# Optimization experiments

Measured on AMD Instinct MI355X. Metric: run time of the kernel, lower is better.

## Reference

```python
import jax, jax.numpy as jnp
import numpy as np


def gcn_layer(x, src, dst, W, b, n_dst):
    # DGL GraphConv, norm='both': D_src^{-1/2} pre-norm, sum aggregate, D_dst^{-1/2} post-norm, + bias
    n_src = x.shape[0]
    e_ones = jnp.ones(src.shape[0], dtype=x.dtype)
    deg_out = jnp.clip(jax.ops.segment_sum(e_ones, src, num_segments=n_src), 1.0)
    deg_in = jnp.clip(jax.ops.segment_sum(e_ones, dst, num_segments=n_dst), 1.0)
    h = (x * jax.lax.rsqrt(deg_out)[:, None]) @ W          # [n_src, out]
    agg = jax.ops.segment_sum(h[src], dst, num_segments=n_dst)  # [n_dst, out]
    return jax.nn.relu(agg * jax.lax.rsqrt(deg_in)[:, None] + b)


def setup_inputs() -> dict:
    key = jax.random.key(0)
    ks = jax.random.split(key, 8)
    N_SRC0, N_DST0, N_DST1 = 400000, 40000, 4000
    E0, E1 = 400000, 40000
    D_IN, D_HID, D_OUT = 256, 256, 256
    x = jax.random.normal(ks[0], (N_SRC0, D_IN), dtype=jnp.float32)
    src0 = jax.random.randint(ks[1], (E0,), 0, N_SRC0)
    dst0 = jax.random.randint(ks[2], (E0,), 0, N_DST0)
    src1 = jax.random.randint(ks[3], (E1,), 0, N_DST0)
    dst1 = jax.random.randint(ks[4], (E1,), 0, N_DST1)
    W0 = jax.random.normal(ks[5], (D_IN, D_HID), dtype=jnp.float32) * (1.0 / np.sqrt(D_IN))
    W1 = jax.random.normal(ks[6], (D_HID, D_OUT), dtype=jnp.float32) * (1.0 / np.sqrt(D_HID))
    b0 = jnp.zeros((D_HID,), dtype=jnp.float32)
    b1 = jnp.zeros((D_OUT,), dtype=jnp.float32)
    return {"x": x, "src0": src0, "dst0": dst0, "src1": src1, "dst1": dst1,
            "W0": W0, "b0": b0, "W1": W1, "b1": b1,
            "n_dst0": N_DST0, "n_dst1": N_DST1}


def reference(x, src0, dst0, src1, dst1, W0, b0, W1, b1, n_dst0, n_dst1):
    h = gcn_layer(x, src0, dst0, W0, b0, n_dst0)   # [n_dst0, hidden]
    out = gcn_layer(h, src1, dst1, W1, b1, n_dst1)  # [n_dst1, out]
    return out
```

## Files before the change

kernel.cpp:

```cpp
#include <hip/hip_runtime.h>
#include <hip/hip_bf16.h>
#include <cstddef>
#include <cstdint>


#define D 256
#define N_DST0_CONST 40000

typedef __attribute__((ext_vector_type(8))) short s16x8;
typedef __attribute__((ext_vector_type(4))) short s16x4;
typedef __attribute__((ext_vector_type(4))) float f32x4;

__device__ inline short f2bf(float f) {
    __hip_bfloat16 h = __float2bfloat16(f);
    return *reinterpret_cast<short*>(&h);
}

__global__ void zero_i(int* __restrict__ p, int n) {
    int i = blockIdx.x * blockDim.x + threadIdx.x;
    int stride = gridDim.x * blockDim.x;
    for (; i < n; i += stride) p[i] = 0;
}

__global__ void count_deg(const int* __restrict__ src, const int* __restrict__ dst,
                          int* __restrict__ cnt_src, int* __restrict__ cnt_dst, int E) {
    int e = blockIdx.x * blockDim.x + threadIdx.x;
    if (e < E) {
        atomicAdd(&cnt_src[src[e]], 1);
        atomicAdd(&cnt_dst[dst[e]], 1);
    }
}

__global__ void finalize_rsqrt(const int* __restrict__ cnt, float* __restrict__ rnorm, int n) {
    int i = blockIdx.x * blockDim.x + threadIdx.x;
    if (i < n) rnorm[i] = rsqrtf(fmaxf((float)cnt[i], 1.0f));
}

__global__ __launch_bounds__(1024) void ex_scan(const int* __restrict__ cnt,
                                                int* __restrict__ ptr, int n) {
    __shared__ int wsum[16];
    const int tid = threadIdx.x;
    const int chunk = (n + 1023) / 1024;
    const int begin = tid * chunk;
    const int end = min(begin + chunk, n);
    int local = 0;
    for (int i = begin; i < end; ++i) local += cnt[i];
    const int lane = tid & 63;
    const int wid = tid >> 6;
    int v = local;
    for (int off = 1; off < 64; off <<= 1) {
        int u = __shfl_up(v, off, 64);
        if (lane >= off) v += u;
    }
    if (lane == 63) wsum[wid] = v;
    __syncthreads();
    if (wid == 0 && lane < 16) {
        int w = wsum[lane];
        for (int off = 1; off < 16; off <<= 1) {
            int u = __shfl_up(w, off, 16);
            if (lane >= off) w += u;
        }
        wsum[lane] = w;
    }
    __syncthreads();
    int base = (wid > 0 ? wsum[wid - 1] : 0) + (v - local);
    int run = base;
    for (int i = begin; i < end; ++i) { ptr[i] = run; run += cnt[i]; }
}

__global__ void fill_csr(const int* __restrict__ src, const int* __restrict__ dst,
                         int* __restrict__ ptr, int* __restrict__ edge_src, int E) {
    int e = blockIdx.x * blockDim.x + threadIdx.x;
    if (e < E) {
        int pos = atomicAdd(&ptr[dst[e]], 1);
        edge_src[pos] = src[e];
    }
}

__global__ __launch_bounds__(256) void gather_agg_bf16(
    const float* __restrict__ X, const int* __restrict__ edge_src,
    const int* __restrict__ ptr, const float* __restrict__ rnorm_src,
    short* __restrict__ agg, int nrows) {
    int d = blockIdx.x * 4 + threadIdx.y;
    if (d >= nrows) return;
    int beg = (d == 0) ? 0 : ptr[d - 1];
    int end = ptr[d];
    int lane = threadIdx.x;
    float4 acc = make_float4(0.f, 0.f, 0.f, 0.f);
    for (int j = beg; j < end; ++j) {
        int s = edge_src[j];
        float sc = rnorm_src[s];
        float4 v = *(const float4*)(X + (size_t)s * D + lane * 4);
        acc.x += v.x * sc;
        acc.y += v.y * sc;
        acc.z += v.z * sc;
        acc.w += v.w * sc;
    }
    s16x4 o;
    o.x = f2bf(acc.x); o.y = f2bf(acc.y); o.z = f2bf(acc.z); o.w = f2bf(acc.w);
    *(s16x4*)(agg + (size_t)d * D + lane * 4) = o;
}

__global__ __launch_bounds__(256) void transpose_cast_w(const float* __restrict__ W,
                                                        short* __restrict__ BT) {
    __shared__ float t[16][17];
    int k0 = blockIdx.x * 16, n0 = blockIdx.y * 16;
    t[threadIdx.y][threadIdx.x] = W[(size_t)(k0 + threadIdx.y) * D + n0 + threadIdx.x];
    __syncthreads();
    BT[(size_t)(n0 + threadIdx.y) * D + k0 + threadIdx.x] = f2bf(t[threadIdx.x][threadIdx.y]);
}

#define LDK 40

__global__ __launch_bounds__(256) void gemm_bf16_mfma(
    const short* __restrict__ A, const short* __restrict__ BT,
    const float* __restrict__ rnorm, const float* __restrict__ bias,
    float* __restrict__ out, int M) {
    __shared__ short As[128][LDK];
    __shared__ short Bs[128][LDK];

    const int tid = threadIdx.x;
    const int m0 = blockIdx.x * 128;
    const int n0 = blockIdx.y * 128;
    const int wave = tid >> 6;
    const int lane = tid & 63;
    const int l15 = lane & 15;
    const int quad = lane >> 4;
    const int mo = (wave & 1) * 64;
    const int no = (wave >> 1) * 64;

    f32x4 acc[4][4] = {};

    for (int k0 = 0; k0 < D; k0 += 32) {
#pragma unroll
        for (int i = 0; i < 2; ++i) {
            int idx = tid + i * 256;
            int row = idx >> 2;
            int kg = (idx & 3) * 8;
            int gm = m0 + row;
            s16x8 av = {};
            if (gm < M) av = *(const s16x8*)(A + (size_t)gm * D + k0 + kg);
            *(s16x8*)&As[row][kg] = av;
            s16x8 bv = *(const s16x8*)(BT + (size_t)(n0 + row) * D + k0 + kg);
            *(s16x8*)&Bs[row][kg] = bv;
        }
        __syncthreads();

        s16x8 af[4], bf[4];
#pragma unroll
        for (int mt = 0; mt < 4; ++mt)
            af[mt] = *(const s16x8*)&As[mo + mt * 16 + l15][quad * 8];
#pragma unroll
        for (int nt = 0; nt < 4; ++nt)
            bf[nt] = *(const s16x8*)&Bs[no + nt * 16 + l15][quad * 8];
#pragma unroll
        for (int mt = 0; mt < 4; ++mt)
#pragma unroll
            for (int nt = 0; nt < 4; ++nt)
                acc[mt][nt] = __builtin_amdgcn_mfma_f32_16x16x32_bf16(
                    af[mt], bf[nt], acc[mt][nt], 0, 0, 0);
        __syncthreads();
    }

#pragma unroll
    for (int mt = 0; mt < 4; ++mt) {
#pragma unroll
        for (int r = 0; r < 4; ++r) {
            int gm = m0 + mo + mt * 16 + quad * 4 + r;
            if (gm >= M) continue;
            float sc = rnorm[gm];
#pragma unroll
            for (int nt = 0; nt < 4; ++nt) {
                int gn = n0 + no + nt * 16 + l15;
                float v = fmaxf(acc[mt][nt][r] * sc + bias[gn], 0.f);
                out[(size_t)gm * D + gn] = v;
            }
        }
    }
}


extern "C" void kernel_launch(void* const* d_in, const int* in_sizes, int n_in,
                              void* d_out, int out_size, void* d_ws, size_t ws_size,
                              hipStream_t stream) {
    const float* x    = (const float*)d_in[0];
    const int*   src0 = (const int*)d_in[1];
    const int*   dst0 = (const int*)d_in[2];
    const int*   src1 = (const int*)d_in[3];
    const int*   dst1 = (const int*)d_in[4];
    const float* W0   = (const float*)d_in[5];
    const float* b0   = (const float*)d_in[6];
    const float* W1   = (const float*)d_in[7];
    const float* b1   = (const float*)d_in[8];

    const int n_src0 = in_sizes[0] / D;
    const int E0     = in_sizes[1];
    const int E1     = in_sizes[3];
    const int n_dst0 = N_DST0_CONST;
    const int n_dst1 = out_size / D;

    char* base = (char*)d_ws;
    size_t off = 0;
    auto alloc = [&](size_t bytes) { void* p = base + off; off = (off + bytes + 63) & ~(size_t)63; return p; };

    int* icnt = (int*)alloc((size_t)(n_src0 + 2 * n_dst0 + n_dst1) * 4);
    int* icnt_src0 = icnt;
    int* icnt_dst0 = icnt + n_src0;
    int* icnt_src1 = icnt + n_src0 + n_dst0;
    int* icnt_dst1 = icnt + n_src0 + 2 * n_dst0;
    const int cnt_total = n_src0 + 2 * n_dst0 + n_dst1;

    int* ptr0      = (int*)alloc((size_t)n_dst0 * 4);
    int* ptr1      = (int*)alloc((size_t)n_dst1 * 4);
    int* edge_src0 = (int*)alloc((size_t)E0 * 4);
    int* edge_src1 = (int*)alloc((size_t)E1 * 4);

    float* rnorm = (float*)alloc((size_t)cnt_total * 4);
    float* rnorm_src0 = rnorm;
    float* rnorm_dst0 = rnorm + n_src0;
    float* rnorm_src1 = rnorm + n_src0 + n_dst0;
    float* rnorm_dst1 = rnorm + n_src0 + 2 * (size_t)n_dst0;

    float* h0    = (float*)alloc((size_t)n_dst0 * D * 4);
    short* aggb0 = (short*)alloc((size_t)n_dst0 * D * 2);
    short* aggb1 = (short*)alloc((size_t)n_dst1 * D * 2);
    short* BT0   = (short*)alloc((size_t)D * D * 2);
    short* BT1   = (short*)alloc((size_t)D * D * 2);

    float* out = (float*)d_out;

    zero_i<<<512, 256, 0, stream>>>(icnt, cnt_total);

    count_deg<<<(E0 + 255) / 256, 256, 0, stream>>>(src0, dst0, icnt_src0, icnt_dst0, E0);
    count_deg<<<(E1 + 255) / 256, 256, 0, stream>>>(src1, dst1, icnt_src1, icnt_dst1, E1);

    finalize_rsqrt<<<(cnt_total + 255) / 256, 256, 0, stream>>>(icnt, rnorm, cnt_total);

    ex_scan<<<1, 1024, 0, stream>>>(icnt_dst0, ptr0, n_dst0);
    ex_scan<<<1, 1024, 0, stream>>>(icnt_dst1, ptr1, n_dst1);

    fill_csr<<<(E0 + 255) / 256, 256, 0, stream>>>(src0, dst0, ptr0, edge_src0, E0);
    fill_csr<<<(E1 + 255) / 256, 256, 0, stream>>>(src1, dst1, ptr1, edge_src1, E1);

    {
        dim3 g(D / 16, D / 16), b(16, 16);
        transpose_cast_w<<<g, b, 0, stream>>>(W0, BT0);
        transpose_cast_w<<<g, b, 0, stream>>>(W1, BT1);
    }

    {
        dim3 blk(64, 4);
        gather_agg_bf16<<<(n_dst0 + 3) / 4, blk, 0, stream>>>(x, edge_src0, ptr0, rnorm_src0, aggb0, n_dst0);
        dim3 grid((n_dst0 + 127) / 128, D / 128);
        gemm_bf16_mfma<<<grid, 256, 0, stream>>>(aggb0, BT0, rnorm_dst0, b0, h0, n_dst0);
    }

    {
        dim3 blk(64, 4);
        gather_agg_bf16<<<(n_dst1 + 3) / 4, blk, 0, stream>>>(h0, edge_src1, ptr1, rnorm_src1, aggb1, n_dst1);
        dim3 grid((n_dst1 + 127) / 128, D / 128);
        gemm_bf16_mfma<<<grid, 256, 0, stream>>>(aggb1, BT1, rnorm_dst1, b1, out, n_dst1);
    }
}
```

Baseline: 728.6 us.

## Merge setup kernels across layers and batch neighbor gathers with lane-shuffled indices

The per-layer degree counting, scan, CSR fill and weight transpose launches are merged into single launches that cover both layers, and the separate rsqrt finalize kernel is removed by computing the norms inline from the counts. The gather kernel now loads up to 64 edge indices and their norms cooperatively, broadcasts them with shuffles, and issues four row loads per iteration to raise memory-level parallelism. This trims launch count and the dependent index-then-norm load chain per edge. The cost is some recomputed rsqrt and a slower fallback path for rows with more than 64 edges.

```diff
diff --git a/kernel.cpp b/kernel.cpp
--- a/kernel.cpp
+++ b/kernel.cpp
@@ -22,26 +22,32 @@
     for (; i < n; i += stride) p[i] = 0;
 }
 
-__global__ void count_deg(const int* __restrict__ src, const int* __restrict__ dst,
-                          int* __restrict__ cnt_src, int* __restrict__ cnt_dst, int E) {
+__global__ void count_deg_both(const int* __restrict__ src0, const int* __restrict__ dst0, int E0,
+                               const int* __restrict__ src1, const int* __restrict__ dst1, int E1,
+                               int* __restrict__ cs0, int* __restrict__ cd0,
+                               int* __restrict__ cs1, int* __restrict__ cd1) {
     int e = blockIdx.x * blockDim.x + threadIdx.x;
-    if (e < E) {
-        atomicAdd(&cnt_src[src[e]], 1);
-        atomicAdd(&cnt_dst[dst[e]], 1);
-    }
-}
-
-__global__ void finalize_rsqrt(const int* __restrict__ cnt, float* __restrict__ rnorm, int n) {
-    int i = blockIdx.x * blockDim.x + threadIdx.x;
-    if (i < n) rnorm[i] = rsqrtf(fmaxf((float)cnt[i], 1.0f));
-}
-
-__global__ __launch_bounds__(1024) void ex_scan(const int* __restrict__ cnt,
-                                                int* __restrict__ ptr, int n) {
+    if (e < E0) {
+        atomicAdd(&cs0[src0[e]], 1);
+        atomicAdd(&cd0[dst0[e]], 1);
+    } else if (e < E0 + E1) {
+        int i = e - E0;
+        atomicAdd(&cs1[src1[i]], 1);
+        atomicAdd(&cd1[dst1[i]], 1);
+    }
+}
+
+__global__ __launch_bounds__(1024) void ex_scan_both(
+    const int* __restrict__ cnt0, int* __restrict__ ptr0, int n0,
+    const int* __restrict__ cnt1, int* __restrict__ ptr1, int n1) {
+    const int* cnt = (blockIdx.x == 0) ? cnt0 : cnt1;
+    int* ptr = (blockIdx.x == 0) ? ptr0 : ptr1;
+    int n = (blockIdx.x == 0) ? n0 : n1;
+
     __shared__ int wsum[16];
     const int tid = threadIdx.x;
     const int chunk = (n + 1023) / 1024;
-    const int begin = tid * chunk;
+    const int begin = min(tid * chunk, n);
     const int end = min(begin + chunk, n);
     int local = 0;
     for (int i = begin; i < end; ++i) local += cnt[i];
@@ -68,41 +74,79 @@
     for (int i = begin; i < end; ++i) { ptr[i] = run; run += cnt[i]; }
 }
 
-__global__ void fill_csr(const int* __restrict__ src, const int* __restrict__ dst,
-                         int* __restrict__ ptr, int* __restrict__ edge_src, int E) {
+__global__ void fill_csr_both(const int* __restrict__ src0, const int* __restrict__ dst0, int E0,
+                              const int* __restrict__ src1, const int* __restrict__ dst1, int E1,
+                              int* __restrict__ ptr0, int* __restrict__ es0,
+                              int* __restrict__ ptr1, int* __restrict__ es1) {
     int e = blockIdx.x * blockDim.x + threadIdx.x;
-    if (e < E) {
-        int pos = atomicAdd(&ptr[dst[e]], 1);
-        edge_src[pos] = src[e];
+    if (e < E0) {
+        int pos = atomicAdd(&ptr0[dst0[e]], 1);
+        es0[pos] = src0[e];
+    } else if (e < E0 + E1) {
+        int i = e - E0;
+        int pos = atomicAdd(&ptr1[dst1[i]], 1);
+        es1[pos] = src1[i];
     }
 }
 
 __global__ __launch_bounds__(256) void gather_agg_bf16(
     const float* __restrict__ X, const int* __restrict__ edge_src,
-    const int* __restrict__ ptr, const float* __restrict__ rnorm_src,
+    const int* __restrict__ ptr, const int* __restrict__ cnt_src,
     short* __restrict__ agg, int nrows) {
     int d = blockIdx.x * 4 + threadIdx.y;
     if (d >= nrows) return;
     int beg = (d == 0) ? 0 : ptr[d - 1];
     int end = ptr[d];
+    int deg = end - beg;
     int lane = threadIdx.x;
+
+    int s_l = 0;
+    float rn_l = 0.f;
+    if (lane < deg) {
+        s_l = edge_src[beg + lane];
+        rn_l = rsqrtf(fmaxf((float)cnt_src[s_l], 1.0f));
+    }
+
     float4 acc = make_float4(0.f, 0.f, 0.f, 0.f);
-    for (int j = beg; j < end; ++j) {
-        int s = edge_src[j];
-        float sc = rnorm_src[s];
+    int nb = min(deg, 64);
+    int j = 0;
+    for (; j + 4 <= nb; j += 4) {
+        int s0 = __shfl(s_l, j + 0), s1 = __shfl(s_l, j + 1);
+        int s2 = __shfl(s_l, j + 2), s3 = __shfl(s_l, j + 3);
+        float r0 = __shfl(rn_l, j + 0), r1 = __shfl(rn_l, j + 1);
+        float r2 = __shfl(rn_l, j + 2), r3 = __shfl(rn_l, j + 3);
+        float4 v0 = *(const float4*)(X + (size_t)s0 * D + lane * 4);
+        float4 v1 = *(const float4*)(X + (size_t)s1 * D + lane * 4);
+        float4 v2 = *(const float4*)(X + (size_t)s2 * D + lane * 4);
+        float4 v3 = *(const float4*)(X + (size_t)s3 * D + lane * 4);
+        acc.x += v0.x * r0 + v1.x * r1 + v2.x * r2 + v3.x * r3;
+        acc.y += v0.y * r0 + v1.y * r1 + v2.y * r2 + v3.y * r3;
+        acc.z += v0.z * r0 + v1.z * r1 + v2.z * r2 + v3.z * r3;
+        acc.w += v0.w * r0 + v1.w * r1 + v2.w * r2 + v3.w * r3;
+    }
+    for (; j < nb; ++j) {
+        int s = __shfl(s_l, j);
+        float r = __shfl(rn_l, j);
         float4 v = *(const float4*)(X + (size_t)s * D + lane * 4);
-        acc.x += v.x * sc;
-        acc.y += v.y * sc;
-        acc.z += v.z * sc;
-        acc.w += v.w * sc;
-    }
+        acc.x += v.x * r; acc.y += v.y * r; acc.z += v.z * r; acc.w += v.w * r;
+    }
+    for (int jj = beg + 64; jj < end; ++jj) {
+        int s = edge_src[jj];
+        float r = rsqrtf(fmaxf((float)cnt_src[s], 1.0f));
+        float4 v = *(const float4*)(X + (size_t)s * D + lane * 4);
+        acc.x += v.x * r; acc.y += v.y * r; acc.z += v.z * r; acc.w += v.w * r;
+    }
+
     s16x4 o;
     o.x = f2bf(acc.x); o.y = f2bf(acc.y); o.z = f2bf(acc.z); o.w = f2bf(acc.w);
     *(s16x4*)(agg + (size_t)d * D + lane * 4) = o;
 }
 
-__global__ __launch_bounds__(256) void transpose_cast_w(const float* __restrict__ W,
-                                                        short* __restrict__ BT) {
+__global__ __launch_bounds__(256) void transpose_cast_w_both(
+    const float* __restrict__ Wa, short* __restrict__ BTa,
+    const float* __restrict__ Wb, short* __restrict__ BTb) {
+    const float* W = (blockIdx.z == 0) ? Wa : Wb;
+    short* BT = (blockIdx.z == 0) ? BTa : BTb;
     __shared__ float t[16][17];
     int k0 = blockIdx.x * 16, n0 = blockIdx.y * 16;
     t[threadIdx.y][threadIdx.x] = W[(size_t)(k0 + threadIdx.y) * D + n0 + threadIdx.x];
@@ -114,7 +158,7 @@
 
 __global__ __launch_bounds__(256) void gemm_bf16_mfma(
     const short* __restrict__ A, const short* __restrict__ BT,
-    const float* __restrict__ rnorm, const float* __restrict__ bias,
+    const int* __restrict__ cnt_dst, const float* __restrict__ bias,
     float* __restrict__ out, int M) {
     __shared__ short As[128][LDK];
     __shared__ short Bs[128][LDK];
@@ -168,7 +212,7 @@
         for (int r = 0; r < 4; ++r) {
             int gm = m0 + mo + mt * 16 + quad * 4 + r;
             if (gm >= M) continue;
-            float sc = rnorm[gm];
+            float sc = rsqrtf(fmaxf((float)cnt_dst[gm], 1.0f));
 #pragma unroll
             for (int nt = 0; nt < 4; ++nt) {
                 int gn = n0 + no + nt * 16 + l15;
@@ -215,12 +259,6 @@
     int* edge_src0 = (int*)alloc((size_t)E0 * 4);
     int* edge_src1 = (int*)alloc((size_t)E1 * 4);
 
-    float* rnorm = (float*)alloc((size_t)cnt_total * 4);
-    float* rnorm_src0 = rnorm;
-    float* rnorm_dst0 = rnorm + n_src0;
-    float* rnorm_src1 = rnorm + n_src0 + n_dst0;
-    float* rnorm_dst1 = rnorm + n_src0 + 2 * (size_t)n_dst0;
-
     float* h0    = (float*)alloc((size_t)n_dst0 * D * 4);
     short* aggb0 = (short*)alloc((size_t)n_dst0 * D * 2);
     short* aggb1 = (short*)alloc((size_t)n_dst1 * D * 2);
@@ -231,34 +269,30 @@
 
     zero_i<<<512, 256, 0, stream>>>(icnt, cnt_total);
 
-    count_deg<<<(E0 + 255) / 256, 256, 0, stream>>>(src0, dst0, icnt_src0, icnt_dst0, E0);
-    count_deg<<<(E1 + 255) / 256, 256, 0, stream>>>(src1, dst1, icnt_src1, icnt_dst1, E1);
-
-    finalize_rsqrt<<<(cnt_total + 255) / 256, 256, 0, stream>>>(icnt, rnorm, cnt_total);
-
-    ex_scan<<<1, 1024, 0, stream>>>(icnt_dst0, ptr0, n_dst0);
-    ex_scan<<<1, 1024, 0, stream>>>(icnt_dst1, ptr1, n_dst1);
-
-    fill_csr<<<(E0 + 255) / 256, 256, 0, stream>>>(src0, dst0, ptr0, edge_src0, E0);
-    fill_csr<<<(E1 + 255) / 256, 256, 0, stream>>>(src1, dst1, ptr1, edge_src1, E1);
+    count_deg_both<<<(E0 + E1 + 255) / 256, 256, 0, stream>>>(
+        src0, dst0, E0, src1, dst1, E1, icnt_src0, icnt_dst0, icnt_src1, icnt_dst1);
+
+    ex_scan_both<<<2, 1024, 0, stream>>>(icnt_dst0, ptr0, n_dst0, icnt_dst1, ptr1, n_dst1);
+
+    fill_csr_both<<<(E0 + E1 + 255) / 256, 256, 0, stream>>>(
+        src0, dst0, E0, src1, dst1, E1, ptr0, edge_src0, ptr1, edge_src1);
 
     {
-        dim3 g(D / 16, D / 16), b(16, 16);
-        transpose_cast_w<<<g, b, 0, stream>>>(W0, BT0);
-        transpose_cast_w<<<g, b, 0, stream>>>(W1, BT1);
+        dim3 g(D / 16, D / 16, 2), b(16, 16);
+        transpose_cast_w_both<<<g, b, 0, stream>>>(W0, BT0, W1, BT1);
     }
 
     {
         dim3 blk(64, 4);
-        gather_agg_bf16<<<(n_dst0 + 3) / 4, blk, 0, stream>>>(x, edge_src0, ptr0, rnorm_src0, aggb0, n_dst0);
+        gather_agg_bf16<<<(n_dst0 + 3) / 4, blk, 0, stream>>>(x, edge_src0, ptr0, icnt_src0, aggb0, n_dst0);
         dim3 grid((n_dst0 + 127) / 128, D / 128);
-        gemm_bf16_mfma<<<grid, 256, 0, stream>>>(aggb0, BT0, rnorm_dst0, b0, h0, n_dst0);
+        gemm_bf16_mfma<<<grid, 256, 0, stream>>>(aggb0, BT0, icnt_dst0, b0, h0, n_dst0);
     }
 
     {
         dim3 blk(64, 4);
-        gather_agg_bf16<<<(n_dst1 + 3) / 4, blk, 0, stream>>>(h0, edge_src1, ptr1, rnorm_src1, aggb1, n_dst1);
+        gather_agg_bf16<<<(n_dst1 + 3) / 4, blk, 0, stream>>>(h0, edge_src1, ptr1, icnt_src1, aggb1, n_dst1);
         dim3 grid((n_dst1 + 127) / 128, D / 128);
-        gemm_bf16_mfma<<<grid, 256, 0, stream>>>(aggb1, BT1, rnorm_dst1, b1, out, n_dst1);
-    }
-}
+        gemm_bf16_mfma<<<grid, 256, 0, stream>>>(aggb1, BT1, icnt_dst1, b1, out, n_dst1);
+    }
+}
```

After: 697.1 us. -4.3%, faster.
